# Kernel optimization log

Hardware: AMD Instinct MI355X
Metric: run time of the kernel (lower is better)

The kernel has to match this reference:

```python
import jax, jax.numpy as jnp
import numpy as np

HIDDEN = 1024
HEADS = 16
HEAD_DIM = HIDDEN // HEADS


def setup_inputs() -> dict:
    key = jax.random.key(0)
    ks = jax.random.split(key, 9)
    s = 1.0 / np.sqrt(HIDDEN)
    inp = {
        "x": jax.random.normal(ks[0], (2, 2048, HIDDEN), dtype=jnp.float32),
        "Wq": jax.random.uniform(ks[1], (HIDDEN, HIDDEN), jnp.float32, -s, s),
        "bq": jax.random.uniform(ks[2], (HIDDEN,), jnp.float32, -s, s),
        "Wk": jax.random.uniform(ks[3], (HIDDEN, HIDDEN), jnp.float32, -s, s),
        "bk": jax.random.uniform(ks[4], (HIDDEN,), jnp.float32, -s, s),
        "Wv": jax.random.uniform(ks[5], (HIDDEN, HIDDEN), jnp.float32, -s, s),
        "bv": jax.random.uniform(ks[6], (HIDDEN,), jnp.float32, -s, s),
        "Wo": jax.random.uniform(ks[7], (HIDDEN, HIDDEN), jnp.float32, -s, s),
        "bo": jax.random.uniform(ks[8], (HIDDEN,), jnp.float32, -s, s),
    }
    return inp


def reference(x, Wq, bq, Wk, bk, Wv, bv, Wo, bo):
    B, S, _ = x.shape
    # QKV projections; reshape to [B, H, S, D]
    def heads(t):
        return t.reshape(B, S, HEADS, HEAD_DIM).transpose(0, 2, 1, 3)
    q = heads(x @ Wq + bq)
    k = heads(x @ Wk + bk)
    v = heads(x @ Wv + bv)
    scale = 1.0 / np.sqrt(HEAD_DIM)
    scores = jnp.einsum('bhqd,bhkd->bhqk', q, k) * scale  # [B,H,S,S]
    attn = jax.nn.softmax(scores, axis=-1)
    out = jnp.einsum('bhqk,bhkd->bhqd', attn, v)  # [B,H,S,D]
    out = out.transpose(0, 2, 1, 3).reshape(B, S, HIDDEN)
    return out @ Wo + bo
```

## Files before the change

### kernel.cpp

```cpp
#include <hip/hip_runtime.h>
#include <math.h>


namespace {

constexpr int kHID = 1024;
constexpr int kNH  = 16;
constexpr int kHD  = 64;
constexpr int kSEQ = 2048;

constexpr float kQScale = 0.125f * 1.4426950408889634f;

typedef unsigned short ushortT;
typedef __attribute__((ext_vector_type(8))) short   bf16x8;
typedef __attribute__((ext_vector_type(4))) float   f32x4;
typedef __attribute__((ext_vector_type(4))) unsigned short u16x4;

#define MFMA(a, b, c) __builtin_amdgcn_mfma_f32_16x16x32_bf16((a), (b), (c), 0, 0, 0)

typedef const __attribute__((address_space(1))) void GVoid;
typedef __attribute__((address_space(3))) void SVoid;

__device__ __forceinline__ void gload_lds16(const ushortT* g, ushortT* l) {
    __builtin_amdgcn_global_load_lds((GVoid*)g, (SVoid*)l, 16, 0, 0);
}

__device__ __forceinline__ ushortT f2bf(float f) {
    unsigned u = __builtin_bit_cast(unsigned, f);
    u += 0x7fffu + ((u >> 16) & 1u);
    return (ushortT)(u >> 16);
}

__device__ __forceinline__ unsigned cvt_pk_bf16(float a, float b) {
    unsigned r;
    asm("v_cvt_pk_bf16_f32 %0, %1, %2" : "=v"(r) : "v"(a), "v"(b));
    return r;
}

__device__ __forceinline__ float4 ld4f(const float* p) { return *reinterpret_cast<const float4*>(p); }

__global__ __launch_bounds__(256) void cvtx_kernel(const float* __restrict__ x,
                                                   ushortT* __restrict__ xb) {
    const size_t i = ((size_t)blockIdx.x * 256 + threadIdx.x) * 4;
    const float4 f = ld4f(&x[i]);
    u16x4 o = { f2bf(f.x), f2bf(f.y), f2bf(f.z), f2bf(f.w) };
    *reinterpret_cast<u16x4*>(&xb[i]) = o;
}

__global__ __launch_bounds__(256) void transw_kernel(
    const float* __restrict__ W0, const float* __restrict__ W1,
    const float* __restrict__ W2, const float* __restrict__ W3,
    ushortT* __restrict__ WtAll) {
    __shared__ ushortT T[64 * 72];
    const float* W = (blockIdx.z == 0) ? W0 : (blockIdx.z == 1) ? W1 : (blockIdx.z == 2) ? W2 : W3;
    ushortT* Wt = WtAll + (size_t)blockIdx.z * kHID * kHID;
    const int kb = blockIdx.y * 64, nb = blockIdx.x * 64;
    const int tid = threadIdx.x;
    {
        const int kr = tid >> 2, nc = (tid & 3) * 16;
        #pragma unroll
        for (int i = 0; i < 16; i += 4) {
            const float4 f = ld4f(&W[(size_t)(kb + kr) * kHID + nb + nc + i]);
            T[kr * 72 + nc + i + 0] = f2bf(f.x);
            T[kr * 72 + nc + i + 1] = f2bf(f.y);
            T[kr * 72 + nc + i + 2] = f2bf(f.z);
            T[kr * 72 + nc + i + 3] = f2bf(f.w);
        }
    }
    __syncthreads();
    {
        const int nr = tid >> 2, kc = (tid & 3) * 16;
        ushortT tmp[16];
        #pragma unroll
        for (int i = 0; i < 16; ++i) tmp[i] = T[(kc + i) * 72 + nr];
        *reinterpret_cast<bf16x8*>(&Wt[(size_t)(nb + nr) * kHID + kb + kc]) =
            *reinterpret_cast<bf16x8*>(&tmp[0]);
        *reinterpret_cast<bf16x8*>(&Wt[(size_t)(nb + nr) * kHID + kb + kc + 8]) =
            *reinterpret_cast<bf16x8*>(&tmp[8]);
    }
}

template <typename Epi>
__device__ __forceinline__ void gemm128_body(
    const ushortT* __restrict__ A, const ushortT* __restrict__ Bt,
    int rowBase, int colBase, ushortT* As, ushortT* Bs, Epi&& epi) {
    const int tid = threadIdx.x, wid = tid >> 6, lane = tid & 63;
    const int hi = lane >> 4, lo = lane & 15;
    const int wr = wid >> 1, wc = wid & 1;
    const int r8 = lane >> 3, jc = lane & 7;

    const f32x4 z4 = {0.f, 0.f, 0.f, 0.f};
    f32x4 acc[4][4];
    #pragma unroll
    for (int mi = 0; mi < 4; ++mi)
        #pragma unroll
        for (int ni = 0; ni < 4; ++ni) acc[mi][ni] = z4;

    auto STAGE = [&](int buf, int k0) {
        #pragma unroll
        for (int i = 0; i < 4; ++i) {
            const int chunk = wid * 4 + i;
            const int row = chunk * 8 + r8;
            const int c8 = 8 * (jc ^ r8);
            gload_lds16(&A [(size_t)(rowBase + row) * kHID + k0 + c8], &As[buf * 8192 + chunk * 512]);
            gload_lds16(&Bt[(size_t)(colBase + row) * kHID + k0 + c8], &Bs[buf * 8192 + chunk * 512]);
        }
    };

    STAGE(0, 0);
    __syncthreads();
    int cur = 0;

    for (int k0 = 0; k0 < kHID; k0 += 64) {
        if (k0 + 64 < kHID) STAGE(cur ^ 1, k0 + 64);

        __builtin_amdgcn_s_setprio(1);
        #pragma unroll
        for (int ks = 0; ks < 2; ++ks) {
            bf16x8 af[4], bfr[4];
            #pragma unroll
            for (int mi = 0; mi < 4; ++mi) {
                const int row = 64 * wr + 16 * mi + lo;
                af[mi] = *reinterpret_cast<const bf16x8*>(
                    &As[cur * 8192 + row * 64 + 8 * ((4 * ks + hi) ^ (row & 7))]);
            }
            #pragma unroll
            for (int ni = 0; ni < 4; ++ni) {
                const int row = 64 * wc + 16 * ni + lo;
                bfr[ni] = *reinterpret_cast<const bf16x8*>(
                    &Bs[cur * 8192 + row * 64 + 8 * ((4 * ks + hi) ^ (row & 7))]);
            }
            #pragma unroll
            for (int mi = 0; mi < 4; ++mi)
                #pragma unroll
                for (int ni = 0; ni < 4; ++ni)
                    acc[mi][ni] = MFMA(af[mi], bfr[ni], acc[mi][ni]);
        }
        __builtin_amdgcn_s_setprio(0);

        __syncthreads();
        cur ^= 1;
    }

    epi(acc, wr, wc, hi, lo);
}

__global__ __launch_bounds__(256, 2) void qkv_mfma_gemm(
    const ushortT* __restrict__ A, const ushortT* __restrict__ WtAll,
    const float* __restrict__ bq, const float* __restrict__ bk, const float* __restrict__ bv,
    ushortT* __restrict__ qkvb) {
    __shared__ ushortT As[2 * 8192];
    __shared__ ushortT Bs[2 * 8192];

    const int z = blockIdx.z;
    const ushortT* Bt = WtAll + (size_t)z * kHID * kHID;
    const float* bias = (z == 0) ? bq : (z == 1) ? bk : bv;
    ushortT* out = qkvb + (size_t)z * 2 * kNH * kSEQ * kHD;
    const float scale = (z == 0) ? kQScale : 1.0f;
    const int rowBase = blockIdx.y * 128, colBase = blockIdx.x * 128;

    gemm128_body(A, Bt, rowBase, colBase, As, Bs,
        [&](f32x4 (&acc)[4][4], int wr, int wc, int hi, int lo) {
            #pragma unroll
            for (int ni = 0; ni < 4; ++ni) {
                const int col = colBase + 64 * wc + 16 * ni + lo;
                const float bcol = bias[col];
                const int h = col >> 6, d = col & 63;
                #pragma unroll
                for (int mi = 0; mi < 4; ++mi)
                    #pragma unroll
                    for (int r = 0; r < 4; ++r) {
                        const int m = rowBase + 64 * wr + 16 * mi + 4 * hi + r;
                        const int b = m >> 11, s = m & (kSEQ - 1);
                        const ushortT val = f2bf((acc[mi][ni][r] + bcol) * scale);
                        if (z == 2)
                            out[(((size_t)b * kNH + h) * kHD + d) * kSEQ + s] = val;
                        else
                            out[(((size_t)b * kNH + h) * kSEQ + s) * kHD + d] = val;
                    }
            }
        });
}

__global__ __launch_bounds__(256, 2) void out_mfma_gemm(
    const ushortT* __restrict__ A, const ushortT* __restrict__ Bt,
    const float* __restrict__ bias, float* __restrict__ out) {
    __shared__ ushortT As[2 * 8192];
    __shared__ ushortT Bs[2 * 8192];

    const int rowBase = blockIdx.y * 128, colBase = blockIdx.x * 128;

    gemm128_body(A, Bt, rowBase, colBase, As, Bs,
        [&](f32x4 (&acc)[4][4], int wr, int wc, int hi, int lo) {
            #pragma unroll
            for (int ni = 0; ni < 4; ++ni) {
                const int col = colBase + 64 * wc + 16 * ni + lo;
                const float bcol = bias[col];
                #pragma unroll
                for (int mi = 0; mi < 4; ++mi)
                    #pragma unroll
                    for (int r = 0; r < 4; ++r) {
                        const int m = rowBase + 64 * wr + 16 * mi + 4 * hi + r;
                        out[(size_t)m * kHID + col] = acc[mi][ni][r] + bcol;
                    }
            }
        });
}

__global__ __launch_bounds__(256, 4) void flash_mfma_kernel(
    const ushortT* __restrict__ Qb, const ushortT* __restrict__ Kb,
    const ushortT* __restrict__ Vtg, ushortT* __restrict__ Ob) {
    __shared__ ushortT Ks[2][64 * 64];
    __shared__ ushortT Vs[2][64 * 64];

    const int tid = threadIdx.x, wid = tid >> 6, lane = tid & 63;
    const int hi = lane >> 4, lo = lane & 15;
    const int h = blockIdx.x;
    const int q0 = blockIdx.y * 64;
    const size_t headBase = ((size_t)blockIdx.z * kNH + h) * (size_t)(kSEQ * kHD);
    const ushortT* Kg = Kb + headBase;
    const ushortT* Vg = Vtg + headBase;

    bf16x8 qf[2];
    #pragma unroll
    for (int c = 0; c < 2; ++c)
        qf[c] = *reinterpret_cast<const bf16x8*>(
            &Qb[headBase + (size_t)(q0 + 16 * wid + lo) * kHD + 32 * c + 8 * hi]);

    const short one = (short)0x3F80;
    const bf16x8 ones = {one, one, one, one, one, one, one, one};

    const f32x4 z4 = {0.f, 0.f, 0.f, 0.f};
    f32x4 acc[4] = {z4, z4, z4, z4};
    f32x4 accL = z4;

    const int r8 = lane >> 3, jc = lane & 7;

    const int kap0 = 8 * (lo >> 2) + (lo & 3);
    const int sk = (lo & 3) | (((lo >> 2) & 1) << 2);
    const int kx0 = (8 * hi) ^ (sk << 3);
    const int kx1 = (32 + 8 * hi) ^ (sk << 3);
    const int sv = (lo & 3) | (((lo >> 3) & 1) << 2);

    auto STAGE = [&](int buf, int kv0) {
        #pragma unroll
        for (int i = 0; i < 2; ++i) {
            const int rowBase = (i * 4 + wid) * 8;
            const int row = rowBase + r8;
            const int s8 = (r8 & 3) | ((wid & 1) << 2);
            gload_lds16(&Kg[(size_t)(kv0 + row) * kHD + 8 * (jc ^ s8)], &Ks[buf][rowBase * 64]);
            gload_lds16(&Vg[(size_t)row * kSEQ + kv0 + 8 * (jc ^ s8)], &Vs[buf][rowBase * 64]);
        }
    };

    STAGE(0, 0);
    __syncthreads();
    int cur = 0;

    for (int t = 0; t < kSEQ / 64; ++t) {
        if (t + 1 < kSEQ / 64) STAGE(cur ^ 1, (t + 1) * 64);

        f32x4 sc[4];
        __builtin_amdgcn_s_setprio(1);
        #pragma unroll
        for (int f = 0; f < 4; ++f) {
            const int kap = kap0 + 4 * (f & 1) + 32 * (f >> 1);
            const bf16x8 kf0 = *reinterpret_cast<const bf16x8*>(&Ks[cur][kap * 64 + kx0]);
            const bf16x8 kf1 = *reinterpret_cast<const bf16x8*>(&Ks[cur][kap * 64 + kx1]);
            sc[f] = MFMA(kf1, qf[1], MFMA(kf0, qf[0], z4));
        }
        __builtin_amdgcn_s_setprio(0);

        float p[4][4];
        #pragma unroll
        for (int f = 0; f < 4; ++f)
            #pragma unroll
            for (int r = 0; r < 4; ++r) p[f][r] = exp2f(sc[f][r]);

        union U { unsigned u[4]; bf16x8 v; };
        U pa0, pa1;
        pa0.u[0] = cvt_pk_bf16(p[0][0], p[0][1]);
        pa0.u[1] = cvt_pk_bf16(p[0][2], p[0][3]);
        pa0.u[2] = cvt_pk_bf16(p[1][0], p[1][1]);
        pa0.u[3] = cvt_pk_bf16(p[1][2], p[1][3]);
        pa1.u[0] = cvt_pk_bf16(p[2][0], p[2][1]);
        pa1.u[1] = cvt_pk_bf16(p[2][2], p[2][3]);
        pa1.u[2] = cvt_pk_bf16(p[3][0], p[3][1]);
        pa1.u[3] = cvt_pk_bf16(p[3][2], p[3][3]);

        __builtin_amdgcn_s_setprio(1);
        accL = MFMA(pa0.v, ones, accL);
        accL = MFMA(pa1.v, ones, accL);
        #pragma unroll
        for (int n = 0; n < 4; ++n) {
            const int vrow = 16 * n + lo;
            const bf16x8 vf0 = *reinterpret_cast<const bf16x8*>(
                &Vs[cur][vrow * 64 + ((8 * hi) ^ (sv << 3))]);
            const bf16x8 vf1 = *reinterpret_cast<const bf16x8*>(
                &Vs[cur][vrow * 64 + ((32 + 8 * hi) ^ (sv << 3))]);
            acc[n] = MFMA(pa0.v, vf0, acc[n]);
            acc[n] = MFMA(pa1.v, vf1, acc[n]);
        }
        __builtin_amdgcn_s_setprio(0);

        __syncthreads();
        cur ^= 1;
    }

    #pragma unroll
    for (int r = 0; r < 4; ++r) {
        const float inv = 1.0f / accL[r];
        const int s = q0 + 16 * wid + 4 * hi + r;
        const size_t base = ((size_t)blockIdx.z * kSEQ + s) * kHID + (size_t)h * kHD;
        #pragma unroll
        for (int n = 0; n < 4; ++n)
            Ob[base + 16 * n + lo] = f2bf(acc[n][r] * inv);
    }
}

}

extern "C" void kernel_launch(void* const* d_in, const int* in_sizes, int n_in,
                              void* d_out, int out_size, void* d_ws, size_t ws_size,
                              hipStream_t stream) {
    (void)in_sizes; (void)n_in; (void)out_size;
    const float* x  = (const float*)d_in[0];
    const float* Wq = (const float*)d_in[1];
    const float* bq = (const float*)d_in[2];
    const float* Wk = (const float*)d_in[3];
    const float* bk = (const float*)d_in[4];
    const float* Wv = (const float*)d_in[5];
    const float* bv = (const float*)d_in[6];
    const float* Wo = (const float*)d_in[7];
    const float* bo = (const float*)d_in[8];

    constexpr size_t kXE = (size_t)2 * kSEQ * kHID;
    constexpr size_t kWE = (size_t)kHID * kHID;
    const size_t needed = (kXE + 4 * kWE + 3 * kXE + kXE) * sizeof(ushortT);
    if (ws_size < needed) return;

    ushortT* xb    = (ushortT*)d_ws;
    ushortT* WtAll = xb + kXE;
    ushortT* qkvb  = WtAll + 4 * kWE;
    ushortT* attnb = qkvb + 3 * kXE;

    const ushortT* qb  = qkvb;
    const ushortT* kb  = qkvb + kXE;
    const ushortT* vtb = qkvb + 2 * kXE;

    cvtx_kernel<<<dim3((unsigned)(kXE / (256 * 4))), 256, 0, stream>>>(x, xb);
    transw_kernel<<<dim3(16, 16, 4), 256, 0, stream>>>(Wq, Wk, Wv, Wo, WtAll);

    qkv_mfma_gemm<<<dim3(8, 32, 3), 256, 0, stream>>>(xb, WtAll, bq, bk, bv, qkvb);

    flash_mfma_kernel<<<dim3(kNH, kSEQ / 64, 2), 256, 0, stream>>>(qb, kb, vtb, attnb);

    out_mfma_gemm<<<dim3(8, 32), 256, 0, stream>>>(attnb, WtAll + 3 * kWE, bo, (float*)d_out);
}
```

Measured before the change: 134.9 us.

## Split KV columns across waves in flash attention, reduce partial outputs via LDS

Restructures the flash attention kernel so each wave processes all 64 query rows against its own 16-key slice of each KV tile, instead of owning 16 query rows. K fragments are loaded once per wave per tile and reused across four query blocks. Two KV tiles are paired so P spans 32 keys per MFMA, and V uses a triple buffer. Row sums are accumulated with scalar adds instead of ones-MFMAs, and partial outputs are reduced across waves through LDS at the end. In exchange it raises register pressure (launch bounds drop to 2 blocks per SM), adds an extra barrier per pair of tiles, and adds a serialized epilogue reduction.

New measurement: 147.9 us. 9.6% more time.

```diff
diff --git a/kernel.cpp b/kernel.cpp
--- a/kernel.cpp
+++ b/kernel.cpp
@@ -13,6 +13,7 @@
 
 typedef unsigned short ushortT;
 typedef __attribute__((ext_vector_type(8))) short   bf16x8;
+typedef __attribute__((ext_vector_type(4))) short   bf16x4;
 typedef __attribute__((ext_vector_type(4))) float   f32x4;
 typedef __attribute__((ext_vector_type(4))) unsigned short u16x4;
 
@@ -207,11 +208,11 @@
         });
 }
 
-__global__ __launch_bounds__(256, 4) void flash_mfma_kernel(
+__global__ __launch_bounds__(256, 2) void flash_mfma_kernel(
     const ushortT* __restrict__ Qb, const ushortT* __restrict__ Kb,
     const ushortT* __restrict__ Vtg, ushortT* __restrict__ Ob) {
     __shared__ ushortT Ks[2][64 * 64];
-    __shared__ ushortT Vs[2][64 * 64];
+    __shared__ ushortT Vs[3][64 * 64];
 
     const int tid = threadIdx.x, wid = tid >> 6, lane = tid & 63;
     const int hi = lane >> 4, lo = lane & 15;
@@ -221,100 +222,154 @@
     const ushortT* Kg = Kb + headBase;
     const ushortT* Vg = Vtg + headBase;
 
-    bf16x8 qf[2];
+    bf16x8 qf[4][2];
     #pragma unroll
-    for (int c = 0; c < 2; ++c)
-        qf[c] = *reinterpret_cast<const bf16x8*>(
-            &Qb[headBase + (size_t)(q0 + 16 * wid + lo) * kHD + 32 * c + 8 * hi]);
-
-    const short one = (short)0x3F80;
-    const bf16x8 ones = {one, one, one, one, one, one, one, one};
+    for (int qb = 0; qb < 4; ++qb)
+        #pragma unroll
+        for (int c = 0; c < 2; ++c)
+            qf[qb][c] = *reinterpret_cast<const bf16x8*>(
+                &Qb[headBase + (size_t)(q0 + 16 * qb + lo) * kHD + 32 * c + 8 * hi]);
 
     const f32x4 z4 = {0.f, 0.f, 0.f, 0.f};
-    f32x4 acc[4] = {z4, z4, z4, z4};
-    f32x4 accL = z4;
+    f32x4 acc[4][4];
+    #pragma unroll
+    for (int qb = 0; qb < 4; ++qb)
+        #pragma unroll
+        for (int n = 0; n < 4; ++n) acc[qb][n] = z4;
+    float l_[4] = {0.f, 0.f, 0.f, 0.f};
 
     const int r8 = lane >> 3, jc = lane & 7;
 
-    const int kap0 = 8 * (lo >> 2) + (lo & 3);
-    const int sk = (lo & 3) | (((lo >> 2) & 1) << 2);
-    const int kx0 = (8 * hi) ^ (sk << 3);
-    const int kx1 = (32 + 8 * hi) ^ (sk << 3);
-    const int sv = (lo & 3) | (((lo >> 3) & 1) << 2);
-
-    auto STAGE = [&](int buf, int kv0) {
+    const int sRow = (lo & 3) | (((lo >> 3) & 1) << 2);
+    const int krow64 = (16 * wid + lo) * 64;
+    const int kx0 = (8 * hi) ^ (sRow << 3);
+    const int kx1 = (32 + 8 * hi) ^ (sRow << 3);
+    const int vxc = (16 * wid + 4 * hi) ^ (sRow << 3);
+
+    union PU { unsigned u[4]; bf16x8 v; };
+    union VU { bf16x4 h[2]; bf16x8 v; };
+    PU pa[4];
+
+    auto STAGE = [&](int kbuf, int vbuf, int kv0) {
         #pragma unroll
         for (int i = 0; i < 2; ++i) {
             const int rowBase = (i * 4 + wid) * 8;
             const int row = rowBase + r8;
             const int s8 = (r8 & 3) | ((wid & 1) << 2);
-            gload_lds16(&Kg[(size_t)(kv0 + row) * kHD + 8 * (jc ^ s8)], &Ks[buf][rowBase * 64]);
-            gload_lds16(&Vg[(size_t)row * kSEQ + kv0 + 8 * (jc ^ s8)], &Vs[buf][rowBase * 64]);
+            gload_lds16(&Kg[(size_t)(kv0 + row) * kHD + 8 * (jc ^ s8)], &Ks[kbuf][rowBase * 64]);
+            gload_lds16(&Vg[(size_t)row * kSEQ + kv0 + 8 * (jc ^ s8)], &Vs[vbuf][rowBase * 64]);
         }
     };
 
-    STAGE(0, 0);
+    STAGE(0, 0, 0);
     __syncthreads();
-    int cur = 0;
-
-    for (int t = 0; t < kSEQ / 64; ++t) {
-        if (t + 1 < kSEQ / 64) STAGE(cur ^ 1, (t + 1) * 64);
-
-        f32x4 sc[4];
-        __builtin_amdgcn_s_setprio(1);
-        #pragma unroll
-        for (int f = 0; f < 4; ++f) {
-            const int kap = kap0 + 4 * (f & 1) + 32 * (f >> 1);
-            const bf16x8 kf0 = *reinterpret_cast<const bf16x8*>(&Ks[cur][kap * 64 + kx0]);
-            const bf16x8 kf1 = *reinterpret_cast<const bf16x8*>(&Ks[cur][kap * 64 + kx1]);
-            sc[f] = MFMA(kf1, qf[1], MFMA(kf0, qf[0], z4));
-        }
-        __builtin_amdgcn_s_setprio(0);
-
-        float p[4][4];
-        #pragma unroll
-        for (int f = 0; f < 4; ++f)
-            #pragma unroll
-            for (int r = 0; r < 4; ++r) p[f][r] = exp2f(sc[f][r]);
-
-        union U { unsigned u[4]; bf16x8 v; };
-        U pa0, pa1;
-        pa0.u[0] = cvt_pk_bf16(p[0][0], p[0][1]);
-        pa0.u[1] = cvt_pk_bf16(p[0][2], p[0][3]);
-        pa0.u[2] = cvt_pk_bf16(p[1][0], p[1][1]);
-        pa0.u[3] = cvt_pk_bf16(p[1][2], p[1][3]);
-        pa1.u[0] = cvt_pk_bf16(p[2][0], p[2][1]);
-        pa1.u[1] = cvt_pk_bf16(p[2][2], p[2][3]);
-        pa1.u[2] = cvt_pk_bf16(p[3][0], p[3][1]);
-        pa1.u[3] = cvt_pk_bf16(p[3][2], p[3][3]);
-
-        __builtin_amdgcn_s_setprio(1);
-        accL = MFMA(pa0.v, ones, accL);
-        accL = MFMA(pa1.v, ones, accL);
-        #pragma unroll
-        for (int n = 0; n < 4; ++n) {
-            const int vrow = 16 * n + lo;
-            const bf16x8 vf0 = *reinterpret_cast<const bf16x8*>(
-                &Vs[cur][vrow * 64 + ((8 * hi) ^ (sv << 3))]);
-            const bf16x8 vf1 = *reinterpret_cast<const bf16x8*>(
-                &Vs[cur][vrow * 64 + ((32 + 8 * hi) ^ (sv << 3))]);
-            acc[n] = MFMA(pa0.v, vf0, acc[n]);
-            acc[n] = MFMA(pa1.v, vf1, acc[n]);
-        }
-        __builtin_amdgcn_s_setprio(0);
-
+
+    for (int i = 0; i < kSEQ / 128; ++i) {
+        const int t0 = 2 * i, t1 = 2 * i + 1;
+
+        STAGE((t0 + 1) & 1, (t0 + 1) % 3, (t0 + 1) * 64);
+        {
+            const ushortT* kbse = &Ks[t0 & 1][0];
+            const bf16x8 kf0 = *reinterpret_cast<const bf16x8*>(&kbse[krow64 + kx0]);
+            const bf16x8 kf1 = *reinterpret_cast<const bf16x8*>(&kbse[krow64 + kx1]);
+            f32x4 sc[4];
+            __builtin_amdgcn_s_setprio(1);
+            #pragma unroll
+            for (int qb = 0; qb < 4; ++qb)
+                sc[qb] = MFMA(kf1, qf[qb][1], MFMA(kf0, qf[qb][0], z4));
+            __builtin_amdgcn_s_setprio(0);
+            #pragma unroll
+            for (int qb = 0; qb < 4; ++qb) {
+                const float p0 = exp2f(sc[qb][0]), p1 = exp2f(sc[qb][1]);
+                const float p2 = exp2f(sc[qb][2]), p3 = exp2f(sc[qb][3]);
+                l_[qb] += (p0 + p1) + (p2 + p3);
+                pa[qb].u[0] = cvt_pk_bf16(p0, p1);
+                pa[qb].u[1] = cvt_pk_bf16(p2, p3);
+            }
+        }
         __syncthreads();
-        cur ^= 1;
+
+        if (t1 + 1 < kSEQ / 64) STAGE((t1 + 1) & 1, (t1 + 1) % 3, (t1 + 1) * 64);
+        {
+            const ushortT* kbso = &Ks[t1 & 1][0];
+            const bf16x8 kf0 = *reinterpret_cast<const bf16x8*>(&kbso[krow64 + kx0]);
+            const bf16x8 kf1 = *reinterpret_cast<const bf16x8*>(&kbso[krow64 + kx1]);
+            f32x4 sc[4];
+            __builtin_amdgcn_s_setprio(1);
+            #pragma unroll
+            for (int qb = 0; qb < 4; ++qb)
+                sc[qb] = MFMA(kf1, qf[qb][1], MFMA(kf0, qf[qb][0], z4));
+            __builtin_amdgcn_s_setprio(0);
+            #pragma unroll
+            for (int qb = 0; qb < 4; ++qb) {
+                const float p0 = exp2f(sc[qb][0]), p1 = exp2f(sc[qb][1]);
+                const float p2 = exp2f(sc[qb][2]), p3 = exp2f(sc[qb][3]);
+                l_[qb] += (p0 + p1) + (p2 + p3);
+                pa[qb].u[2] = cvt_pk_bf16(p0, p1);
+                pa[qb].u[3] = cvt_pk_bf16(p2, p3);
+            }
+        }
+        {
+            const ushortT* ve = &Vs[t0 % 3][0];
+            const ushortT* vo = &Vs[t1 % 3][0];
+            __builtin_amdgcn_s_setprio(1);
+            #pragma unroll
+            for (int n = 0; n < 4; ++n) {
+                const int off = (16 * n + lo) * 64 + vxc;
+                VU vu;
+                vu.h[0] = *reinterpret_cast<const bf16x4*>(&ve[off]);
+                vu.h[1] = *reinterpret_cast<const bf16x4*>(&vo[off]);
+                #pragma unroll
+                for (int qb = 0; qb < 4; ++qb)
+                    acc[qb][n] = MFMA(pa[qb].v, vu.v, acc[qb][n]);
+            }
+            __builtin_amdgcn_s_setprio(0);
+        }
+        __syncthreads();
     }
 
+    float* MK = reinterpret_cast<float*>(&Ks[0][0]);
+    float* ML = reinterpret_cast<float*>(&Vs[0][0]);
+
     #pragma unroll
-    for (int r = 0; r < 4; ++r) {
-        const float inv = 1.0f / accL[r];
-        const int s = q0 + 16 * wid + 4 * hi + r;
-        const size_t base = ((size_t)blockIdx.z * kSEQ + s) * kHID + (size_t)h * kHD;
-        #pragma unroll
-        for (int n = 0; n < 4; ++n)
-            Ob[base + 16 * n + lo] = f2bf(acc[n][r] * inv);
+    for (int qb = 0; qb < 4; ++qb) {
+        float lq = l_[qb];
+        lq += __shfl_xor(lq, 16);
+        lq += __shfl_xor(lq, 32);
+
+        if (wid != qb) {
+            #pragma unroll
+            for (int n = 0; n < 4; ++n)
+                *reinterpret_cast<f32x4*>(&MK[wid * 1024 + n * 256 + lane * 4]) = acc[qb][n];
+            if (hi == 0) ML[wid * 16 + lo] = lq;
+        }
+        __syncthreads();
+        if (wid == qb) {
+            float lt = lq;
+            #pragma unroll
+            for (int w = 0; w < 4; ++w)
+                if (w != qb) lt += ML[w * 16 + lo];
+            f32x4 tot[4];
+            #pragma unroll
+            for (int n = 0; n < 4; ++n) tot[n] = acc[qb][n];
+            #pragma unroll
+            for (int w = 0; w < 4; ++w) {
+                if (w == qb) continue;
+                #pragma unroll
+                for (int n = 0; n < 4; ++n)
+                    tot[n] += *reinterpret_cast<const f32x4*>(&MK[w * 1024 + n * 256 + lane * 4]);
+            }
+            #pragma unroll
+            for (int r = 0; r < 4; ++r) {
+                const float inv = 1.0f / __shfl(lt, 4 * hi + r);
+                const int s = q0 + 16 * qb + 4 * hi + r;
+                const size_t base = ((size_t)blockIdx.z * kSEQ + s) * kHID + (size_t)h * kHD;
+                #pragma unroll
+                for (int n = 0; n < 4; ++n)
+                    Ob[base + 16 * n + lo] = f2bf(tot[n][r] * inv);
+            }
+        }
+        __syncthreads();
     }
 }
 
```
